# Optimization experiments

Measured on AMD Instinct MI355X. Metric: run time of the kernel, lower is better.

The kernel has to match this reference:

```python
import jax, jax.numpy as jnp
import numpy as np

L = 2        # n_layer
D = 1024     # hidden_size
H = 8        # n_head
DK = D // H  # head_dim = 128
DV = D // H
T = 2048     # max_seq_length
B = 4
INTER = 2816 # fla GatedMLP: int(1024*4*2/3)=2730 rounded up to multiple of 256
EPS = 1e-6


def rmsnorm(x, w):
    return x * jax.lax.rsqrt(jnp.mean(x * x, axis=-1, keepdims=True) + EPS) * w


def l2norm(x):
    return x * jax.lax.rsqrt(jnp.sum(x * x, axis=-1, keepdims=True) + EPS)


def delta_attn(x, Wq, Wk, Wv, Wb, Wo, onorm_w):
    # x: [B, T, D]
    b, t, _ = x.shape
    q = jax.nn.silu((x @ Wq).reshape(b, t, H, DK))
    k = jax.nn.silu((x @ Wk).reshape(b, t, H, DK))
    q = l2norm(q)
    k = l2norm(k)
    v = jax.nn.silu((x @ Wv).reshape(b, t, H, DV))
    beta = jax.nn.sigmoid(x @ Wb) * 2.0  # [B,T,H], allow_neg_eigval=True
    # time-major for scan
    qt = q.transpose(1, 0, 2, 3)  # [T,B,H,DK]
    kt = k.transpose(1, 0, 2, 3)
    vt = v.transpose(1, 0, 2, 3)
    bt = beta.transpose(1, 0, 2)  # [T,B,H]

    def step(S, inps):
        qi, ki, vi, bi = inps
        # delta rule: S_t = S_{t-1} + beta_t * k_t (v_t - S_{t-1}^T k_t)^T
        pred = jnp.einsum('bhkv,bhk->bhv', S, ki)
        S = S + bi[..., None, None] * ki[..., :, None] * (vi - pred)[..., None, :]
        o = jnp.einsum('bhkv,bhk->bhv', S, qi)
        return S, o

    S0 = jnp.zeros((b, H, DK, DV), x.dtype)
    _, o = jax.lax.scan(step, S0, (qt, kt, vt, bt))  # o: [T,B,H,DV]
    o = rmsnorm(o, onorm_w)  # per-head RMSNorm (use_gate=False)
    o = o.transpose(1, 0, 2, 3).reshape(b, t, H * DV)
    return o @ Wo


def setup_inputs() -> dict:
    key = jax.random.key(0)
    ks = jax.random.split(key, 13)
    s = 0.02
    f32 = jnp.float32
    return {
        'input_embeds': jax.random.normal(ks[0], (T, B, D), f32),
        'Wq': jax.random.normal(ks[1], (L, D, D), f32) * s,
        'Wk': jax.random.normal(ks[2], (L, D, D), f32) * s,
        'Wv': jax.random.normal(ks[3], (L, D, D), f32) * s,
        'Wb': jax.random.normal(ks[4], (L, D, H), f32) * s,
        'Wo': jax.random.normal(ks[5], (L, D, D), f32) * s,
        'onorm_w': jnp.ones((L, DV), f32) + jax.random.normal(ks[6], (L, DV), f32) * 0.02,
        'norm1_w': jnp.ones((L, D), f32) + jax.random.normal(ks[7], (L, D), f32) * 0.02,
        'norm2_w': jnp.ones((L, D), f32) + jax.random.normal(ks[8], (L, D), f32) * 0.02,
        'Wg': jax.random.normal(ks[9], (L, D, 2 * INTER), f32) * s,
        'Wd': jax.random.normal(ks[10], (L, INTER, D), f32) * s,
        'final_norm_w': jnp.ones((D,), f32) + jax.random.normal(ks[11], (D,), f32) * 0.02,
    }


def reference(input_embeds, Wq, Wk, Wv, Wb, Wo, onorm_w, norm1_w, norm2_w, Wg, Wd, final_norm_w):
    # wrapper transposes (T,B,D) -> (B,T,D)
    x = input_embeds.transpose(1, 0, 2)
    for l in range(L):
        h = rmsnorm(x, norm1_w[l])
        x = x + delta_attn(h, Wq[l], Wk[l], Wv[l], Wb[l], Wo[l], onorm_w[l])
        h = rmsnorm(x, norm2_w[l])
        gy = h @ Wg[l]
        g, y = jnp.split(gy, 2, axis=-1)
        x = x + (jax.nn.silu(g) * y) @ Wd[l]
    x = rmsnorm(x, final_norm_w)
    return x.transpose(1, 0, 2)  # back to (T,B,D)
```

## Files before the change

kernel.cpp:

```cpp
#include <hip/hip_runtime.h>
#include <hip/hip_bf16.h>
#include <cstdint>


typedef _Float16 f16;
typedef __attribute__((ext_vector_type(8))) _Float16 h8;
typedef __attribute__((ext_vector_type(4))) _Float16 h4;
typedef __attribute__((ext_vector_type(4))) float f4;

#define DEV __device__ __forceinline__

static constexpr int Bb_ = 4;
static constexpr int Hh  = 8;
static constexpr int Dd  = 1024;
static constexpr int Tt  = 2048;
static constexpr int NC  = 32;

DEV float siluf(float x) { return x / (1.f + expf(-x)); }
DEV int swz16(int row, int c) { return (c & 8) | ((c & 7) ^ (row & 7)); }

#define AS1(p) ((const __attribute__((address_space(1))) void*)(uintptr_t)(p))
#define AS3(p) ((__attribute__((address_space(3))) void*)(uint32_t)(uintptr_t)(p))

DEV h8 rd_sw(const f16* T, int row, int chunk) {
  return *(const h8*)(T + (((row << 3) | (chunk ^ (row & 7))) * 8));
}

template<int EPI, int SC>
__global__ __launch_bounds__(512, 2) void gemm2(const f16* __restrict__ A, const f16* __restrict__ Bt,
                                                void* __restrict__ C, const float* __restrict__ rs,
                                                int M, int N, int K, int gx) {
  __shared__ __align__(16) f16 ldsA[2][16384];
  __shared__ __align__(16) f16 ldsB[2][8192];
  const int tid = threadIdx.x, lane = tid & 63, w = tid >> 6;
  const int l15 = lane & 15, l4 = lane >> 4;
  const int wr = w >> 2, wc = w & 3;
  const int nwg = gridDim.x;
  int flat = blockIdx.x;
  if ((nwg & 7) == 0) flat = (flat & 7) * (nwg >> 3) + (flat >> 3);
  const int bx = flat % gx, by = flat / gx;

  const f16* Ab = A + (size_t)by * 256 * K;
  const f16* Bb = Bt + (size_t)bx * 128 * K;
  const int NT = K >> 6;
  f4 acc[8][2] = {};

  const int r0 = tid >> 3;
  const size_t soff0 = (size_t)r0 * K + (size_t)(((tid & 7) ^ (r0 & 7)) * 8);
  const size_t soff1 = soff0 + (size_t)64 * K;
  const int dof = tid * 8;
  auto STG = [&](const f16* base, f16* dst) {
    __builtin_amdgcn_global_load_lds(AS1(base + soff0), AS3(dst + dof), 16, 0, 0);
    __builtin_amdgcn_global_load_lds(AS1(base + soff1), AS3(dst + 4096 + dof), 16, 0, 0);
  };

  STG(Bb, ldsB[0]);
  STG(Ab, ldsA[0]);
  STG(Ab + (size_t)128 * K, ldsA[0] + 8192);
  if (NT > 1) {
    STG(Bb + 64, ldsB[1]);
    asm volatile("s_waitcnt vmcnt(2)");
  } else {
    asm volatile("s_waitcnt vmcnt(0)");
  }
  __builtin_amdgcn_s_barrier();

  for (int t = 0; t < NT; ++t) {
    const int cur = t & 1, nxt = cur ^ 1;
    const f16* cA = ldsA[cur];
    const f16* cB = ldsB[cur];
    h8 b[2][2], aX[2][2], aY[2][2];
#pragma unroll
    for (int cf = 0; cf < 2; ++cf)
#pragma unroll
      for (int ks = 0; ks < 2; ++ks)
        b[cf][ks] = rd_sw(cB, wc * 32 + cf * 16 + l15, ks * 4 + l4);
#pragma unroll
    for (int fr = 0; fr < 2; ++fr)
#pragma unroll
      for (int ks = 0; ks < 2; ++ks)
        aX[fr][ks] = rd_sw(cA, wr * 128 + fr * 16 + l15, ks * 4 + l4);
    if (t + 1 < NT) { STG(Ab + (t + 1) * 64, ldsA[nxt]); STG(Ab + (size_t)128 * K + (t + 1) * 64, ldsA[nxt] + 8192); }
    __builtin_amdgcn_s_setprio(1);
#pragma unroll
    for (int fr = 0; fr < 2; ++fr)
#pragma unroll
      for (int cf = 0; cf < 2; ++cf)
#pragma unroll
        for (int ks = 0; ks < 2; ++ks)
          acc[fr][cf] = __builtin_amdgcn_mfma_f32_16x16x32_f16(aX[fr][ks], b[cf][ks], acc[fr][cf], 0, 0, 0);
#pragma unroll
    for (int fr = 0; fr < 2; ++fr)
#pragma unroll
      for (int ks = 0; ks < 2; ++ks)
        aY[fr][ks] = rd_sw(cA, wr * 128 + 32 + fr * 16 + l15, ks * 4 + l4);
#pragma unroll
    for (int fr = 0; fr < 2; ++fr)
#pragma unroll
      for (int cf = 0; cf < 2; ++cf)
#pragma unroll
        for (int ks = 0; ks < 2; ++ks)
          acc[2 + fr][cf] = __builtin_amdgcn_mfma_f32_16x16x32_f16(aY[fr][ks], b[cf][ks], acc[2 + fr][cf], 0, 0, 0);
    __builtin_amdgcn_s_setprio(0);
    __builtin_amdgcn_s_barrier();
#pragma unroll
    for (int fr = 0; fr < 2; ++fr)
#pragma unroll
      for (int ks = 0; ks < 2; ++ks)
        aX[fr][ks] = rd_sw(cA, wr * 128 + 64 + fr * 16 + l15, ks * 4 + l4);
    if (t + 2 < NT) STG(Bb + (t + 2) * 64, ldsB[cur]);
    __builtin_amdgcn_s_setprio(1);
#pragma unroll
    for (int fr = 0; fr < 2; ++fr)
#pragma unroll
      for (int cf = 0; cf < 2; ++cf)
#pragma unroll
        for (int ks = 0; ks < 2; ++ks)
          acc[4 + fr][cf] = __builtin_amdgcn_mfma_f32_16x16x32_f16(aX[fr][ks], b[cf][ks], acc[4 + fr][cf], 0, 0, 0);
#pragma unroll
    for (int fr = 0; fr < 2; ++fr)
#pragma unroll
      for (int ks = 0; ks < 2; ++ks)
        aY[fr][ks] = rd_sw(cA, wr * 128 + 96 + fr * 16 + l15, ks * 4 + l4);
#pragma unroll
    for (int fr = 0; fr < 2; ++fr)
#pragma unroll
      for (int cf = 0; cf < 2; ++cf)
#pragma unroll
        for (int ks = 0; ks < 2; ++ks)
          acc[6 + fr][cf] = __builtin_amdgcn_mfma_f32_16x16x32_f16(aY[fr][ks], b[cf][ks], acc[6 + fr][cf], 0, 0, 0);
    __builtin_amdgcn_s_setprio(0);
    if (t + 2 < NT)      asm volatile("s_waitcnt vmcnt(2)" ::: "memory");
    else if (t + 1 < NT) asm volatile("s_waitcnt vmcnt(0)" ::: "memory");
    __builtin_amdgcn_s_barrier();
  }

#pragma unroll
  for (int fr = 0; fr < 8; ++fr) {
#pragma unroll
    for (int cf = 0; cf < 2; ++cf) {
      const int row0 = by * 256 + wr * 128 + fr * 16 + l4 * 4;
      const int col = bx * 128 + wc * 32 + cf * 16 + l15;
#pragma unroll
      for (int q = 0; q < 4; ++q) {
        const size_t idx = (size_t)(row0 + q) * N + col;
        float v = acc[fr][cf][q];
        if (SC) v *= rs[row0 + q];
        if (EPI == 1) ((f16*)C)[idx] = (f16)((float)((f16*)C)[idx] + v);
        if (EPI == 2) ((f16*)C)[idx] = (f16)v;
      }
    }
  }
}

__global__ __launch_bounds__(512, 2) void gemmGLU(const f16* __restrict__ A, const f16* __restrict__ WgT,
                                                  const float* __restrict__ rs, f16* __restrict__ my,
                                                  int K, int gx) {
  __shared__ __align__(16) f16 ldsA[2][16384];
  __shared__ __align__(16) f16 ldsG[2][8192];
  __shared__ __align__(16) f16 ldsY[2][8192];
  const int tid = threadIdx.x, lane = tid & 63, w = tid >> 6;
  const int l15 = lane & 15, l4 = lane >> 4;
  const int wr = w >> 2, wc = w & 3;
  const int nwg = gridDim.x;
  int flat = blockIdx.x;
  if ((nwg & 7) == 0) flat = (flat & 7) * (nwg >> 3) + (flat >> 3);
  const int bx = flat % gx, by = flat / gx;

  const f16* Ab = A + (size_t)by * 256 * K;
  const f16* Gb = WgT + (size_t)bx * 128 * K;
  const f16* Yb = WgT + (size_t)(2816 + bx * 128) * K;
  const int NT = K >> 6;
  f4 accG[8][2] = {}, accY[8][2] = {};

  const int r0 = tid >> 3;
  const size_t soff0 = (size_t)r0 * K + (size_t)(((tid & 7) ^ (r0 & 7)) * 8);
  const size_t soff1 = soff0 + (size_t)64 * K;
  const int dof = tid * 8;
  auto STG = [&](const f16* base, f16* dst) {
    __builtin_amdgcn_global_load_lds(AS1(base + soff0), AS3(dst + dof), 16, 0, 0);
    __builtin_amdgcn_global_load_lds(AS1(base + soff1), AS3(dst + 4096 + dof), 16, 0, 0);
  };

  STG(Gb, ldsG[0]);
  STG(Yb, ldsY[0]);
  STG(Ab, ldsA[0]);
  STG(Ab + (size_t)128 * K, ldsA[0] + 8192);
  if (NT > 1) {
    STG(Gb + 64, ldsG[1]);
    STG(Yb + 64, ldsY[1]);
    asm volatile("s_waitcnt vmcnt(4)");
  } else {
    asm volatile("s_waitcnt vmcnt(0)");
  }
  __builtin_amdgcn_s_barrier();

  for (int t = 0; t < NT; ++t) {
    const int cur = t & 1, nxt = cur ^ 1;
    const f16* cA = ldsA[cur];
    h8 bg[2][2], byv[2][2], aX[2][2], aY[2][2];
#pragma unroll
    for (int cf = 0; cf < 2; ++cf)
#pragma unroll
      for (int ks = 0; ks < 2; ++ks) {
        bg[cf][ks] = rd_sw(ldsG[cur], wc * 32 + cf * 16 + l15, ks * 4 + l4);
        byv[cf][ks] = rd_sw(ldsY[cur], wc * 32 + cf * 16 + l15, ks * 4 + l4);
      }
#pragma unroll
    for (int fr = 0; fr < 2; ++fr)
#pragma unroll
      for (int ks = 0; ks < 2; ++ks)
        aX[fr][ks] = rd_sw(cA, wr * 128 + fr * 16 + l15, ks * 4 + l4);
    if (t + 1 < NT) { STG(Ab + (t + 1) * 64, ldsA[nxt]); STG(Ab + (size_t)128 * K + (t + 1) * 64, ldsA[nxt] + 8192); }
    __builtin_amdgcn_s_setprio(1);
#pragma unroll
    for (int fr = 0; fr < 2; ++fr)
#pragma unroll
      for (int cf = 0; cf < 2; ++cf)
#pragma unroll
        for (int ks = 0; ks < 2; ++ks) {
          accG[fr][cf] = __builtin_amdgcn_mfma_f32_16x16x32_f16(aX[fr][ks], bg[cf][ks], accG[fr][cf], 0, 0, 0);
          accY[fr][cf] = __builtin_amdgcn_mfma_f32_16x16x32_f16(aX[fr][ks], byv[cf][ks], accY[fr][cf], 0, 0, 0);
        }
#pragma unroll
    for (int fr = 0; fr < 2; ++fr)
#pragma unroll
      for (int ks = 0; ks < 2; ++ks)
        aY[fr][ks] = rd_sw(cA, wr * 128 + 32 + fr * 16 + l15, ks * 4 + l4);
#pragma unroll
    for (int fr = 0; fr < 2; ++fr)
#pragma unroll
      for (int cf = 0; cf < 2; ++cf)
#pragma unroll
        for (int ks = 0; ks < 2; ++ks) {
          accG[2 + fr][cf] = __builtin_amdgcn_mfma_f32_16x16x32_f16(aY[fr][ks], bg[cf][ks], accG[2 + fr][cf], 0, 0, 0);
          accY[2 + fr][cf] = __builtin_amdgcn_mfma_f32_16x16x32_f16(aY[fr][ks], byv[cf][ks], accY[2 + fr][cf], 0, 0, 0);
        }
    __builtin_amdgcn_s_setprio(0);
    __builtin_amdgcn_s_barrier();
#pragma unroll
    for (int fr = 0; fr < 2; ++fr)
#pragma unroll
      for (int ks = 0; ks < 2; ++ks)
        aX[fr][ks] = rd_sw(cA, wr * 128 + 64 + fr * 16 + l15, ks * 4 + l4);
    if (t + 2 < NT) { STG(Gb + (t + 2) * 64, ldsG[cur]); STG(Yb + (t + 2) * 64, ldsY[cur]); }
    __builtin_amdgcn_s_setprio(1);
#pragma unroll
    for (int fr = 0; fr < 2; ++fr)
#pragma unroll
      for (int cf = 0; cf < 2; ++cf)
#pragma unroll
        for (int ks = 0; ks < 2; ++ks) {
          accG[4 + fr][cf] = __builtin_amdgcn_mfma_f32_16x16x32_f16(aX[fr][ks], bg[cf][ks], accG[4 + fr][cf], 0, 0, 0);
          accY[4 + fr][cf] = __builtin_amdgcn_mfma_f32_16x16x32_f16(aX[fr][ks], byv[cf][ks], accY[4 + fr][cf], 0, 0, 0);
        }
#pragma unroll
    for (int fr = 0; fr < 2; ++fr)
#pragma unroll
      for (int ks = 0; ks < 2; ++ks)
        aY[fr][ks] = rd_sw(cA, wr * 128 + 96 + fr * 16 + l15, ks * 4 + l4);
#pragma unroll
    for (int fr = 0; fr < 2; ++fr)
#pragma unroll
      for (int cf = 0; cf < 2; ++cf)
#pragma unroll
        for (int ks = 0; ks < 2; ++ks) {
          accG[6 + fr][cf] = __builtin_amdgcn_mfma_f32_16x16x32_f16(aY[fr][ks], bg[cf][ks], accG[6 + fr][cf], 0, 0, 0);
          accY[6 + fr][cf] = __builtin_amdgcn_mfma_f32_16x16x32_f16(aY[fr][ks], byv[cf][ks], accY[6 + fr][cf], 0, 0, 0);
        }
    __builtin_amdgcn_s_setprio(0);
    if (t + 2 < NT)      asm volatile("s_waitcnt vmcnt(4)" ::: "memory");
    else if (t + 1 < NT) asm volatile("s_waitcnt vmcnt(0)" ::: "memory");
    __builtin_amdgcn_s_barrier();
  }

#pragma unroll
  for (int fr = 0; fr < 8; ++fr) {
#pragma unroll
    for (int cf = 0; cf < 2; ++cf) {
      const int row0 = by * 256 + wr * 128 + fr * 16 + l4 * 4;
      const int col = bx * 128 + wc * 32 + cf * 16 + l15;
#pragma unroll
      for (int q = 0; q < 4; ++q) {
        const float s = rs[row0 + q];
        my[(size_t)(row0 + q) * 2816 + col] = (f16)(siluf(s * accG[fr][cf][q]) * (s * accY[fr][cf][q]));
      }
    }
  }
}

__global__ __launch_bounds__(256) void cvt_k(const float* __restrict__ in, f16* __restrict__ out) {
  const size_t i = ((size_t)blockIdx.x * 256 + threadIdx.x) * 8;
  const float4 a = *(const float4*)(in + i);
  const float4 b = *(const float4*)(in + i + 4);
  h8 o = {(f16)a.x, (f16)a.y, (f16)a.z, (f16)a.w, (f16)b.x, (f16)b.y, (f16)b.z, (f16)b.w};
  *(h8*)(out + i) = o;
}

__global__ __launch_bounds__(256) void rowscale_k(const f16* __restrict__ x, float* __restrict__ rs) {
  const int tid = threadIdx.x, lane = tid & 63, wv = tid >> 6;
  const int r = blockIdx.x * 4 + wv;
  const f16* row = x + (size_t)r * 1024 + lane * 16;
  const h8 v0 = *(const h8*)(row);
  const h8 v1 = *(const h8*)(row + 8);
  float ss = 0.f;
#pragma unroll
  for (int e = 0; e < 8; ++e) {
    const float a = (float)v0[e], b = (float)v1[e];
    ss += a * a + b * b;
  }
#pragma unroll
  for (int m = 1; m < 64; m <<= 1) ss += __shfl_xor(ss, m);
  if (lane == 0) rs[r] = rsqrtf(ss * (1.f / 1024.f) + 1e-6f);
}

__global__ __launch_bounds__(256) void rmsnorm_f(const f16* __restrict__ x, const float* __restrict__ w,
                                                 float* __restrict__ out) {
  const int r = blockIdx.x, tid = threadIdx.x;
  const h4 xv = *(const h4*)(x + (size_t)r * 1024 + tid * 4);
  const float v0 = (float)xv[0], v1 = (float)xv[1], v2 = (float)xv[2], v3 = (float)xv[3];
  float ss = v0 * v0 + v1 * v1 + v2 * v2 + v3 * v3;
#pragma unroll
  for (int m = 1; m < 64; m <<= 1) ss += __shfl_xor(ss, m);
  __shared__ float red[4];
  if ((tid & 63) == 0) red[tid >> 6] = ss;
  __syncthreads();
  const float scale = rsqrtf((red[0] + red[1] + red[2] + red[3]) * (1.f / 1024.f) + 1e-6f);
  const float4 w4 = *(const float4*)(w + tid * 4);
  *(float4*)(out + (size_t)r * 1024 + tid * 4) =
      make_float4(v0 * scale * w4.x, v1 * scale * w4.y, v2 * scale * w4.z, v3 * scale * w4.w);
}

__global__ __launch_bounds__(256) void qkv_epi(const f16* __restrict__ qkv, f16* __restrict__ qb,
                                               f16* __restrict__ kb, f16* __restrict__ vb) {
  const int r = blockIdx.x, tid = threadIdx.x;
  const int head = tid >> 5, l32 = tid & 31;
  const int i = (r >> 2) & 63;
  const size_t src = (size_t)r * 3072 + head * 128 + l32 * 4;
  {
    const h4 v = *(const h4*)(qkv + src);
    float s0 = siluf((float)v[0]), s1 = siluf((float)v[1]), s2 = siluf((float)v[2]), s3 = siluf((float)v[3]);
    float ss = s0 * s0 + s1 * s1 + s2 * s2 + s3 * s3;
#pragma unroll
    for (int m = 1; m <= 16; m <<= 1) ss += __shfl_xor(ss, m);
    const float sc = rsqrtf(ss + 1e-6f);
    h4 o = {(f16)(s0 * sc), (f16)(s1 * sc), (f16)(s2 * sc), (f16)(s3 * sc)};
    const int c = l32 >> 1, off = (l32 & 1) * 4;
    *(h4*)(qb + (size_t)r * 1024 + head * 128 + swz16(i, c) * 8 + off) = o;
  }
  {
    const h4 v = *(const h4*)(qkv + src + 1024);
    float s0 = siluf((float)v[0]), s1 = siluf((float)v[1]), s2 = siluf((float)v[2]), s3 = siluf((float)v[3]);
    float ss = s0 * s0 + s1 * s1 + s2 * s2 + s3 * s3;
#pragma unroll
    for (int m = 1; m <= 16; m <<= 1) ss += __shfl_xor(ss, m);
    const float sc = rsqrtf(ss + 1e-6f);
    h4 o = {(f16)(s0 * sc), (f16)(s1 * sc), (f16)(s2 * sc), (f16)(s3 * sc)};
    const int c = l32 >> 1, off = (l32 & 1) * 4;
    *(h4*)(kb + (size_t)r * 1024 + head * 128 + swz16(i, c) * 8 + off) = o;
  }
  {
    const h4 v = *(const h4*)(qkv + (size_t)r * 3072 + 2048 + tid * 4);
    h4 o = {(f16)siluf((float)v[0]), (f16)siluf((float)v[1]), (f16)siluf((float)v[2]), (f16)siluf((float)v[3])};
    const int hd = tid >> 5, dh = (tid & 31) * 4;
    const int c = dh >> 3, off = dh & 7;
    *(h4*)(vb + (size_t)r * 1024 + hd * 128 + swz16(i, c) * 8 + off) = o;
  }
}

__global__ __launch_bounds__(256) void onorm_k(const f16* __restrict__ o, const float* __restrict__ w,
                                               f16* __restrict__ ob) {
  const int r = blockIdx.x, tid = threadIdx.x;
  const int head = tid >> 5, l32 = tid & 31;
  const size_t base = (size_t)r * 1024 + head * 128 + l32 * 4;
  const h4 xv = *(const h4*)(o + base);
  const float v0 = (float)xv[0], v1 = (float)xv[1], v2 = (float)xv[2], v3 = (float)xv[3];
  float ss = v0 * v0 + v1 * v1 + v2 * v2 + v3 * v3;
#pragma unroll
  for (int m = 1; m <= 16; m <<= 1) ss += __shfl_xor(ss, m);
  const float sc = rsqrtf(ss * (1.f / 128.f) + 1e-6f);
  const float4 w4 = *(const float4*)(w + l32 * 4);
  h4 out = {(f16)(v0 * sc * w4.x), (f16)(v1 * sc * w4.y), (f16)(v2 * sc * w4.z), (f16)(v3 * sc * w4.w)};
  *(h4*)(ob + base) = out;
}

__global__ __launch_bounds__(256) void beta_k(const f16* __restrict__ x, const float* __restrict__ Wb2,
                                              const float* __restrict__ rs, float* __restrict__ beta) {
  const int tid = threadIdx.x, lane = tid & 63, wv = tid >> 6;
  const int r = blockIdx.x * 4 + wv;
  const f16* row = x + (size_t)r * 1024 + lane * 16;
  const h8 v0 = *(const h8*)(row);
  const h8 v1 = *(const h8*)(row + 8);
  const float* wb = Wb2 + (size_t)(lane * 16) * 8;
  float acc[8] = {};
#pragma unroll
  for (int e = 0; e < 8; ++e) {
    const float x0 = (float)v0[e], x1 = (float)v1[e];
    const float4 w0a = *(const float4*)(wb + e * 8);
    const float4 w0b = *(const float4*)(wb + e * 8 + 4);
    const float4 w1a = *(const float4*)(wb + (e + 8) * 8);
    const float4 w1b = *(const float4*)(wb + (e + 8) * 8 + 4);
    acc[0] += x0 * w0a.x + x1 * w1a.x;  acc[1] += x0 * w0a.y + x1 * w1a.y;
    acc[2] += x0 * w0a.z + x1 * w1a.z;  acc[3] += x0 * w0a.w + x1 * w1a.w;
    acc[4] += x0 * w0b.x + x1 * w1b.x;  acc[5] += x0 * w0b.y + x1 * w1b.y;
    acc[6] += x0 * w0b.z + x1 * w1b.z;  acc[7] += x0 * w0b.w + x1 * w1b.w;
  }
#pragma unroll
  for (int j = 0; j < 8; ++j)
#pragma unroll
    for (int m = 1; m < 64; m <<= 1) acc[j] += __shfl_xor(acc[j], m);
  if (lane == 0) {
    const float s = rs[r];
#pragma unroll
    for (int j = 0; j < 8; ++j) beta[(size_t)r * 8 + j] = 2.f / (1.f + expf(-acc[j] * s));
  }
}

template<int FOLD>
__global__ __launch_bounds__(256) void transpose_k(const float* __restrict__ W, const float* __restrict__ rw,
                                                   f16* __restrict__ Wt, int K, int N) {
  __shared__ float tile[32][33];
  const int n0 = blockIdx.x * 32, k0 = blockIdx.y * 32;
  const int tx = threadIdx.x & 31, ty = threadIdx.x >> 5;
#pragma unroll
  for (int i = 0; i < 32; i += 8) {
    float v = W[(size_t)(k0 + ty + i) * N + n0 + tx];
    if (FOLD) v *= rw[k0 + ty + i];
    tile[ty + i][tx] = v;
  }
  __syncthreads();
#pragma unroll
  for (int i = 0; i < 32; i += 8) Wt[(size_t)(n0 + ty + i) * K + k0 + tx] = (f16)tile[tx][ty + i];
}

__global__ __launch_bounds__(256) void bweight_k(const float* __restrict__ Wb, const float* __restrict__ n1w,
                                                 float* __restrict__ Wb2) {
  const int idx = blockIdx.x * 256 + threadIdx.x;
  Wb2[idx] = Wb[idx] * n1w[idx >> 3];
}

__global__ void fill_k(float* p, int n, float v) {
  const int i = blockIdx.x * 256 + threadIdx.x;
  if (i < n) p[i] = v;
}

DEV f4 mm16(const f16* A, int as, const f16* B, f4 c, int l15, int l4) {
  h4 a = *(const h4*)(A + l15 * as + l4 * 4);
  h4 b = *(const h4*)(B + l15 * 20 + l4 * 4);
  return __builtin_amdgcn_mfma_f32_16x16x16f16(a, b, c, 0, 0, 0);
}
DEV void wr_T(f16* slot, f4 acc, int l15, int l4, float sgn) {
  h4 v = {(f16)(sgn * acc[0]), (f16)(sgn * acc[1]), (f16)(sgn * acc[2]), (f16)(sgn * acc[3])};
  *(h4*)(slot + l15 * 20 + l4 * 4) = v;
}
DEV void wr_Tb(f16* Tb, int bi, int bj, f4 acc, const float* betas, int l15, int l4, float sgn) {
  const float bc = betas[bj * 16 + l15];
#pragma unroll
  for (int q = 0; q < 4; ++q)
    Tb[(bi * 16 + l4 * 4 + q) * 72 + bj * 16 + l15] = (f16)(sgn * acc[q] * bc);
}

__global__ __launch_bounds__(256) void phaseA(const f16* __restrict__ kb, const f16* __restrict__ qb,
                                              const f16* __restrict__ vb, const float* __restrict__ beta,
                                              f16* __restrict__ wbuf, f16* __restrict__ utbuf,
                                              f16* __restrict__ pbuf, f16* __restrict__ ktbuf) {
  const int blk = blockIdx.x;
  const int c = blk >> 5, bh = blk & 31;
  const int b = bh >> 3, h = bh & 7;
  const int tid = threadIdx.x, lane = tid & 63, wv = tid >> 6;
  const int l15 = lane & 15, l4 = lane >> 4;

  __shared__ __align__(16) f16 Ks[64 * 128];
  __shared__ __align__(16) f16 QVs[64 * 128];
  __shared__ __align__(16) f16 Abuf[64 * 68];
  __shared__ __align__(16) f16 Dr[4][16 * 20];
  __shared__ __align__(16) f16 Dt[4][16 * 20];
  __shared__ __align__(16) f16 Tp[3][16 * 20];
  __shared__ __align__(16) f16 Xp[3][16 * 20];
  __shared__ __align__(16) f16 Tb[64 * 72];
  __shared__ float betas[64];

  const size_t rowstr = (size_t)Bb_ * Dd;
  const size_t gbase = ((size_t)(c * 64) * Bb_ + b) * Dd + h * 128;

#pragma unroll
  for (int i = 0; i < 4; ++i) {
    const int ch = tid + i * 256;
    const int rr = ch >> 4, kc = ch & 15;
    *(h8*)(Ks + ch * 8) = *(const h8*)(kb + gbase + (size_t)rr * rowstr + kc * 8);
    *(h8*)(QVs + ch * 8) = *(const h8*)(qb + gbase + (size_t)rr * rowstr + kc * 8);
  }
  for (int i = tid; i < 64 * 72; i += 256) Tb[i] = (f16)0.f;
  if (tid < 64) betas[tid] = beta[((size_t)(c * 64 + tid) * Bb_ + b) * Hh + h];
  __syncthreads();

  f4 accS[4] = {}, accP[4] = {};
  const int arow = wv * 16 + l15;
#pragma unroll
  for (int kc = 0; kc < 4; ++kc) {
    const int c4 = kc * 4 + l4;
    const h8 aK = *(const h8*)(Ks + arow * 128 + swz16(arow, c4) * 8);
    const h8 aQ = *(const h8*)(QVs + arow * 128 + swz16(arow, c4) * 8);
#pragma unroll
    for (int f = 0; f < 4; ++f) {
      const int brow = f * 16 + l15;
      const h8 bK = *(const h8*)(Ks + brow * 128 + swz16(brow, c4) * 8);
      accS[f] = __builtin_amdgcn_mfma_f32_16x16x32_f16(aK, bK, accS[f], 0, 0, 0);
      accP[f] = __builtin_amdgcn_mfma_f32_16x16x32_f16(aQ, bK, accP[f], 0, 0, 0);
    }
  }
  const size_t pbase = (((size_t)bh * NC + c) * 64) * 64;
#pragma unroll
  for (int f = 0; f < 4; ++f) {
#pragma unroll
    for (int q = 0; q < 4; ++q) {
      const int i = wv * 16 + l4 * 4 + q;
      const int j = f * 16 + l15;
      Abuf[i * 68 + j] = (f16)((j < i) ? betas[i] * accS[f][q] : 0.f);
      pbuf[pbase + (size_t)i * 64 + j] = (f16)((j <= i) ? accP[f][q] : 0.f);
    }
  }
  __syncthreads();

#pragma unroll
  for (int i = 0; i < 4; ++i) {
    const int ch = tid + i * 256;
    const int rr = ch >> 4, kc = ch & 15;
    *(h8*)(QVs + ch * 8) = *(const h8*)(vb + gbase + (size_t)rr * rowstr + kc * 8);
  }

  {
    const int bi = wv;
    const int cc = l15;
    const f16* Ad = Abuf + (bi * 16) * 68 + bi * 16;
    float t[16];
    t[0] = (cc == 0) ? 1.f : 0.f;
#pragma unroll
    for (int i = 1; i < 16; ++i) {
      float s = (cc == i) ? 1.f : 0.f;
#pragma unroll
      for (int j = 0; j < i; ++j) s -= (float)Ad[i * 68 + j] * t[j];
      t[i] = s;
    }
    if (lane < 16) {
#pragma unroll
      for (int j4 = 0; j4 < 4; ++j4) {
        h4 v = {(f16)t[j4 * 4], (f16)t[j4 * 4 + 1], (f16)t[j4 * 4 + 2], (f16)t[j4 * 4 + 3]};
        *(h4*)(&Dt[bi][cc * 20 + j4 * 4]) = v;
      }
      const float bc = betas[bi * 16 + cc];
#pragma unroll
      for (int j = 0; j < 16; ++j) {
        Dr[bi][j * 20 + cc] = (f16)t[j];
        Tb[(bi * 16 + j) * 72 + bi * 16 + cc] = (f16)(t[j] * bc);
      }
    }
  }
  __syncthreads();

  const f16* AB10 = Abuf + 16 * 68 + 0;
  const f16* AB20 = Abuf + 32 * 68 + 0;
  const f16* AB21 = Abuf + 32 * 68 + 16;
  const f16* AB30 = Abuf + 48 * 68 + 0;
  const f16* AB31 = Abuf + 48 * 68 + 16;
  const f16* AB32 = Abuf + 48 * 68 + 32;
  f4 z = {};
  f4 x20, x30;

  if (wv == 0) wr_T(Xp[0], mm16(AB10, 68, Dt[0], z, l15, l4), l15, l4, 1.f);
  if (wv == 1) wr_T(Xp[1], mm16(AB21, 68, Dt[1], z, l15, l4), l15, l4, 1.f);
  if (wv == 2) wr_T(Xp[2], mm16(AB32, 68, Dt[2], z, l15, l4), l15, l4, 1.f);
  if (wv == 3) x20 = mm16(AB20, 68, Dt[0], z, l15, l4);
  __syncthreads();
  if (wv == 0) { f4 r = mm16(Dr[1], 20, Xp[0], z, l15, l4); wr_T(Tp[0], r, l15, l4, -1.f); wr_Tb(Tb, 1, 0, r, betas, l15, l4, -1.f); }
  if (wv == 1) { f4 r = mm16(Dr[2], 20, Xp[1], z, l15, l4); wr_T(Tp[1], r, l15, l4, -1.f); wr_Tb(Tb, 2, 1, r, betas, l15, l4, -1.f); }
  if (wv == 2) { f4 r = mm16(Dr[3], 20, Xp[2], z, l15, l4); wr_Tb(Tb, 3, 2, r, betas, l15, l4, -1.f); }
  if (wv == 3) x30 = mm16(AB30, 68, Dt[0], z, l15, l4);
  __syncthreads();
  if (wv == 3) wr_T(Xp[0], mm16(AB21, 68, Tp[0], x20, l15, l4), l15, l4, 1.f);
  if (wv == 1) { f4 r = mm16(AB31, 68, Dt[1], z, l15, l4); r = mm16(AB32, 68, Tp[1], r, l15, l4); wr_T(Xp[1], r, l15, l4, 1.f); }
  __syncthreads();
  if (wv == 3) { f4 r = mm16(Dr[2], 20, Xp[0], z, l15, l4); wr_T(Tp[2], r, l15, l4, -1.f); wr_Tb(Tb, 2, 0, r, betas, l15, l4, -1.f); }
  if (wv == 1) { f4 r = mm16(Dr[3], 20, Xp[1], z, l15, l4); wr_Tb(Tb, 3, 1, r, betas, l15, l4, -1.f); }
  __syncthreads();
  if (wv == 3) { f4 r = mm16(AB31, 68, Tp[0], x30, l15, l4); r = mm16(AB32, 68, Tp[2], r, l15, l4); wr_T(Xp[2], r, l15, l4, 1.f); }
  __syncthreads();
  if (wv == 3) { f4 r = mm16(Dr[3], 20, Xp[2], z, l15, l4); wr_Tb(Tb, 3, 0, r, betas, l15, l4, -1.f); }
  __syncthreads();

  const size_t wub = ((size_t)bh * NC + c) * 8192;
  const int koff = l4 * 8;
  f4 wacc[8] = {}, uacc[8] = {};
#pragma unroll
  for (int kc = 0; kc < 2; ++kc) {
    const h8 aT = *(const h8*)(Tb + (wv * 16 + l15) * 72 + kc * 32 + koff);
#pragma unroll
    for (int f = 0; f < 8; ++f) {
      const int d = f * 16 + l15, cD = d >> 3, d7 = d & 7;
      h8 bK, bV;
#pragma unroll
      for (int j = 0; j < 8; ++j) {
        const int t2 = kc * 32 + koff + j;
        const int pos = t2 * 128 + swz16(t2, cD) * 8 + d7;
        bK[j] = Ks[pos];
        bV[j] = QVs[pos];
      }
      wacc[f] = __builtin_amdgcn_mfma_f32_16x16x32_f16(aT, bK, wacc[f], 0, 0, 0);
      uacc[f] = __builtin_amdgcn_mfma_f32_16x16x32_f16(aT, bV, uacc[f], 0, 0, 0);
    }
  }
#pragma unroll
  for (int f = 0; f < 8; ++f) {
    const int d = f * 16 + l15, cD = d >> 3, d7 = d & 7;
#pragma unroll
    for (int q = 0; q < 4; ++q) {
      const int i = wv * 16 + l4 * 4 + q;
      wbuf[wub + (size_t)i * 128 + swz16(i, cD) * 8 + d7] = (f16)wacc[f][q];
    }
    h4 uv = {(f16)uacc[f][0], (f16)uacc[f][1], (f16)uacc[f][2], (f16)uacc[f][3]};
    *(h4*)(utbuf + wub + (size_t)d * 64 + wv * 16 + l4 * 4) = uv;
  }

#pragma unroll
  for (int i2 = 0; i2 < 4; ++i2) {
    const int ch = tid + i2 * 256;
    const int dp = ch & 127, c2 = ch >> 7;
    h8 v;
#pragma unroll
    for (int j = 0; j < 8; ++j) {
      const int i = c2 * 8 + j;
      v[j] = Ks[i * 128 + swz16(i, dp >> 3) * 8 + (dp & 7)];
    }
    *(h8*)(ktbuf + wub + (size_t)dp * 64 + (c2 ^ (dp & 7)) * 8) = v;
  }
}

__global__ __launch_bounds__(256) void phaseB(const f16* __restrict__ qb, const f16* __restrict__ ktbuf,
                                              const f16* __restrict__ wbuf, const f16* __restrict__ utbuf,
                                              const f16* __restrict__ pbuf, f16* __restrict__ obuf) {
  const int blk = blockIdx.x;
  const int bh = blk >> 2, g = blk & 3;
  const int b = bh >> 3, h = bh & 7;
  const int tid = threadIdx.x, lane = tid & 63, wv = tid >> 6;
  const int l15 = lane & 15, l4 = lane >> 4;

  __shared__ __align__(16) f16 Ws[2][8192];
  __shared__ __align__(16) f16 Qs[2][8192];
  __shared__ __align__(16) f16 Kts[2][8192];
  __shared__ __align__(16) f16 Rt[32 * 72];
  __shared__ __align__(16) f16 Ms[32 * 136];

  for (int i = tid; i < 32 * 136; i += 256) Ms[i] = (f16)0.f;
  f4 macc[2][2] = {};

  const int arow = wv * 16 + l15;
  const int koff = l4 * 8;

  auto STAGE = [&](int c2, int buf) {
#pragma unroll
    for (int i = 0; i < 4; ++i) {
      const int ch = tid + i * 256;
      const size_t tb = ((size_t)bh * NC + c2) * 8192;
      __builtin_amdgcn_global_load_lds(AS1(wbuf + tb + ch * 8), AS3(Ws[buf] + ch * 8), 16, 0, 0);
      __builtin_amdgcn_global_load_lds(AS1(ktbuf + tb + ch * 8), AS3(Kts[buf] + ch * 8), 16, 0, 0);
      const int rr = ch >> 4, kc2 = ch & 15;
      __builtin_amdgcn_global_load_lds(AS1(qb + ((size_t)((c2 * 64 + rr) * 4 + b)) * 1024 + h * 128 + kc2 * 8),
                                       AS3(Qs[buf] + ch * 8), 16, 0, 0);
    }
  };

  STAGE(0, 0);
  asm volatile("s_waitcnt vmcnt(0)" ::: "memory");
  __builtin_amdgcn_s_barrier();

  for (int c = 0; c < NC; ++c) {
    const int cur = c & 1, nxt = cur ^ 1;
    const size_t pcb = ((size_t)bh * NC + c) * 4096;
    const h8 aP0 = *(const h8*)(pbuf + pcb + arow * 64 + koff);
    const h8 aP1 = *(const h8*)(pbuf + pcb + arow * 64 + 32 + koff);
    const size_t ucb = ((size_t)bh * NC + c) * 8192;
    const h4 u0 = *(const h4*)(utbuf + ucb + (size_t)(g * 32 + l15) * 64 + wv * 16 + l4 * 4);
    const h4 u1 = *(const h4*)(utbuf + ucb + (size_t)(g * 32 + 16 + l15) * 64 + wv * 16 + l4 * 4);
    asm volatile("s_waitcnt vmcnt(4)" ::: "memory");
    asm volatile("s_waitcnt lgkmcnt(0)" ::: "memory");
    __builtin_amdgcn_s_barrier();
    if (c + 1 < NC) STAGE(c + 1, nxt);

    f4 accR[2] = {}, accO[2] = {};
    __builtin_amdgcn_s_setprio(1);
#pragma unroll
    for (int kc = 0; kc < 4; ++kc) {
      const int c4 = kc * 4 + l4;
      const h8 aW = *(const h8*)(Ws[cur] + arow * 128 + swz16(arow, c4) * 8);
      const h8 aQ = *(const h8*)(Qs[cur] + arow * 128 + swz16(arow, c4) * 8);
#pragma unroll
      for (int f = 0; f < 2; ++f) {
        const h8 bM = *(const h8*)(Ms + (f * 16 + l15) * 136 + kc * 32 + koff);
        accR[f] = __builtin_amdgcn_mfma_f32_16x16x32_f16(aW, bM, accR[f], 0, 0, 0);
        accO[f] = __builtin_amdgcn_mfma_f32_16x16x32_f16(aQ, bM, accO[f], 0, 0, 0);
      }
    }
    __builtin_amdgcn_s_setprio(0);
    if (c + 1 < NC) asm volatile("s_waitcnt vmcnt(12)" ::: "memory");
    else            asm volatile("s_waitcnt vmcnt(0)" ::: "memory");
#pragma unroll
    for (int f = 0; f < 2; ++f) {
      const h4 uu = f ? u1 : u0;
      h4 rw;
#pragma unroll
      for (int q = 0; q < 4; ++q) {
        const float rv = (float)uu[q] - accR[f][q];
        accR[f][q] = rv;
        rw[q] = (f16)rv;
      }
      *(h4*)(Rt + (f * 16 + l15) * 72 + wv * 16 + l4 * 4) = rw;
    }
    asm volatile("s_waitcnt lgkmcnt(0)" ::: "memory");
    __builtin_amdgcn_s_barrier();

#pragma unroll
    for (int kc = 0; kc < 2; ++kc) {
      const h8 aP = kc ? aP1 : aP0;
#pragma unroll
      for (int f = 0; f < 2; ++f) {
        const h8 bR = *(const h8*)(Rt + (f * 16 + l15) * 72 + kc * 32 + koff);
        accO[f] = __builtin_amdgcn_mfma_f32_16x16x32_f16(aP, bR, accO[f], 0, 0, 0);
      }
    }
#pragma unroll
    for (int f = 0; f < 2; ++f)
#pragma unroll
      for (int q = 0; q < 4; ++q) {
        const int i = wv * 16 + l4 * 4 + q;
        const int cc = f * 16 + l15;
        obuf[((size_t)(c * 64 + i) * Bb_ + b) * Dd + h * 128 + g * 32 + cc] = (f16)accO[f][q];
      }

#pragma unroll
    for (int kc = 0; kc < 2; ++kc) {
      const h8 aR0 = *(const h8*)(Rt + l15 * 72 + kc * 32 + koff);
      const h8 aR1 = *(const h8*)(Rt + (16 + l15) * 72 + kc * 32 + koff);
#pragma unroll
      for (int cf = 0; cf < 2; ++cf) {
        const int kcol = wv * 32 + cf * 16 + l15;
        const int c2 = kc * 4 + l4;
        const h8 bKv = *(const h8*)(Kts[cur] + kcol * 64 + (c2 ^ (kcol & 7)) * 8);
        macc[0][cf] = __builtin_amdgcn_mfma_f32_16x16x32_f16(aR0, bKv, macc[0][cf], 0, 0, 0);
        macc[1][cf] = __builtin_amdgcn_mfma_f32_16x16x32_f16(aR1, bKv, macc[1][cf], 0, 0, 0);
      }
    }
#pragma unroll
    for (int rf = 0; rf < 2; ++rf)
#pragma unroll
      for (int cf = 0; cf < 2; ++cf)
#pragma unroll
        for (int q = 0; q < 4; ++q) {
          const int cr = rf * 16 + l4 * 4 + q;
          const int kcol = wv * 32 + cf * 16 + l15;
          Ms[cr * 136 + kcol] = (f16)macc[rf][cf][q];
        }
  }
}

extern "C" void kernel_launch(void* const* d_in, const int* in_sizes, int n_in,
                              void* d_out, int out_size, void* d_ws, size_t ws_size,
                              hipStream_t stream) {
  (void)in_sizes; (void)n_in;
  const float* input = (const float*)d_in[0];
  const float* Wq = (const float*)d_in[1];
  const float* Wk = (const float*)d_in[2];
  const float* Wv = (const float*)d_in[3];
  const float* Wb = (const float*)d_in[4];
  const float* Wo = (const float*)d_in[5];
  const float* onw = (const float*)d_in[6];
  const float* n1w = (const float*)d_in[7];
  const float* n2w = (const float*)d_in[8];
  const float* Wg = (const float*)d_in[9];
  const float* Wd = (const float*)d_in[10];
  const float* fnw = (const float*)d_in[11];

  char* ws = (char*)d_ws;
  size_t off = 0;
  auto alloc = [&](size_t bytes) { void* p = ws + off; off += (bytes + 255) & ~(size_t)255; return p; };
  const size_t RD = 8192ull * 1024ull;
  f16*  x     = (f16*)alloc(RD * 2);
  f16*  qb    = (f16*)alloc(RD * 2);
  f16*  kbuf  = (f16*)alloc(RD * 2);
  f16*  vbuf  = (f16*)alloc(RD * 2);
  float* beta = (float*)alloc(8192ull * 8 * 4);
  float* rs   = (float*)alloc(8192ull * 4);
  float* Wb2  = (float*)alloc(1024ull * 8 * 4);
  f16*  wbuf  = (f16*)alloc(RD * 2);
  f16*  utbuf = (f16*)alloc(RD * 2);
  f16*  ktbuf = (f16*)alloc(RD * 2);
  f16*  pbuf  = (f16*)alloc(32ull * 32 * 64 * 64 * 2);
  char* arena = (char*)alloc(3 * RD * 2);
  f16*  WqkvT = (f16*)alloc(3072ull * 1024 * 2);
  f16*  WoT   = (f16*)alloc(1024ull * 1024 * 2);
  f16*  WgT   = (f16*)alloc(5632ull * 1024 * 2);
  f16*  WdT   = (f16*)alloc(1024ull * 2816 * 2);
  if (off > ws_size) {
    fill_k<<<(out_size + 255) / 256, 256, 0, stream>>>((float*)d_out, out_size, 1.0e6f);
    return;
  }
  f16* qkvraw = (f16*)arena;
  f16* obuf = (f16*)arena;
  f16* my = qb;
  f16* ob = wbuf;

  cvt_k<<<4096, 256, 0, stream>>>(input, x);

  for (int l = 0; l < 2; ++l) {
    const size_t o2 = (size_t)l * 1024 * 1024;
    transpose_k<1><<<dim3(32, 32), 256, 0, stream>>>(Wq + o2, n1w + l * 1024, WqkvT, 1024, 1024);
    transpose_k<1><<<dim3(32, 32), 256, 0, stream>>>(Wk + o2, n1w + l * 1024, WqkvT + 1024ull * 1024, 1024, 1024);
    transpose_k<1><<<dim3(32, 32), 256, 0, stream>>>(Wv + o2, n1w + l * 1024, WqkvT + 2048ull * 1024, 1024, 1024);
    transpose_k<0><<<dim3(32, 32), 256, 0, stream>>>(Wo + o2, nullptr, WoT, 1024, 1024);
    transpose_k<1><<<dim3(176, 32), 256, 0, stream>>>(Wg + (size_t)l * 1024 * 5632, n2w + l * 1024, WgT, 1024, 5632);
    transpose_k<0><<<dim3(32, 88), 256, 0, stream>>>(Wd + (size_t)l * 2816 * 1024, nullptr, WdT, 2816, 1024);
    bweight_k<<<32, 256, 0, stream>>>(Wb + (size_t)l * 1024 * 8, n1w + l * 1024, Wb2);

    rowscale_k<<<2048, 256, 0, stream>>>(x, rs);
    gemm2<2, 1><<<32 * 24, 512, 0, stream>>>(x, WqkvT, qkvraw, rs, 8192, 3072, 1024, 24);
    beta_k<<<2048, 256, 0, stream>>>(x, Wb2, rs, beta);
    qkv_epi<<<8192, 256, 0, stream>>>(qkvraw, qb, kbuf, vbuf);
    phaseA<<<1024, 256, 0, stream>>>(kbuf, qb, vbuf, beta, wbuf, utbuf, pbuf, ktbuf);
    phaseB<<<128, 256, 0, stream>>>(qb, ktbuf, wbuf, utbuf, pbuf, obuf);
    onorm_k<<<8192, 256, 0, stream>>>(obuf, onw + l * 128, ob);
    gemm2<1, 0><<<32 * 8, 512, 0, stream>>>(ob, WoT, x, nullptr, 8192, 1024, 1024, 8);

    rowscale_k<<<2048, 256, 0, stream>>>(x, rs);
    gemmGLU<<<32 * 22, 512, 0, stream>>>(x, WgT, rs, my, 1024, 22);
    gemm2<1, 0><<<32 * 8, 512, 0, stream>>>(my, WdT, x, nullptr, 8192, 1024, 2816, 8);
  }
  rmsnorm_f<<<8192, 256, 0, stream>>>(x, fnw, (float*)d_out);
}
```

Baseline: 989.2 us.

## Fuse QKV epilogue into GEMM and split phaseB across more blocks

Adds a gemmQKV kernel that applies row scaling, SiLU, per-head L2 normalization and the swizzled scatter to q/k/v directly in the GEMM epilogue. This removes the separate qkv_epi pass and the raw QKV intermediate round trip through memory. PhaseB now splits each (batch, head) state into 8 column groups of 16 instead of 4 groups of 32, launching 256 blocks instead of 128, with a reordered block index. That raises parallelism in the scan at the cost of recomputing the shared W/Q/P loads per group and doing thinner MFMA work per block.

```diff
diff --git a/kernel.cpp b/kernel.cpp
--- a/kernel.cpp
+++ b/kernel.cpp
@@ -153,6 +153,170 @@
   }
 }
 
+__global__ __launch_bounds__(512, 2) void gemmQKV(const f16* __restrict__ A, const f16* __restrict__ Bt,
+                                                  const float* __restrict__ rs, f16* __restrict__ qb,
+                                                  f16* __restrict__ kb, f16* __restrict__ vb,
+                                                  int K, int gx) {
+  __shared__ __align__(16) f16 ldsA[2][16384];
+  __shared__ __align__(16) f16 ldsB[2][8192];
+  __shared__ float ps[4][256];
+  const int tid = threadIdx.x, lane = tid & 63, w = tid >> 6;
+  const int l15 = lane & 15, l4 = lane >> 4;
+  const int wr = w >> 2, wc = w & 3;
+  const int nwg = gridDim.x;
+  int flat = blockIdx.x;
+  if ((nwg & 7) == 0) flat = (flat & 7) * (nwg >> 3) + (flat >> 3);
+  const int bx = flat % gx, by = flat / gx;
+
+  const f16* Ab = A + (size_t)by * 256 * K;
+  const f16* Bb = Bt + (size_t)bx * 128 * K;
+  const int NT = K >> 6;
+  f4 acc[8][2] = {};
+
+  const int r0 = tid >> 3;
+  const size_t soff0 = (size_t)r0 * K + (size_t)(((tid & 7) ^ (r0 & 7)) * 8);
+  const size_t soff1 = soff0 + (size_t)64 * K;
+  const int dof = tid * 8;
+  auto STG = [&](const f16* base, f16* dst) {
+    __builtin_amdgcn_global_load_lds(AS1(base + soff0), AS3(dst + dof), 16, 0, 0);
+    __builtin_amdgcn_global_load_lds(AS1(base + soff1), AS3(dst + 4096 + dof), 16, 0, 0);
+  };
+
+  STG(Bb, ldsB[0]);
+  STG(Ab, ldsA[0]);
+  STG(Ab + (size_t)128 * K, ldsA[0] + 8192);
+  if (NT > 1) {
+    STG(Bb + 64, ldsB[1]);
+    asm volatile("s_waitcnt vmcnt(2)");
+  } else {
+    asm volatile("s_waitcnt vmcnt(0)");
+  }
+  __builtin_amdgcn_s_barrier();
+
+  for (int t = 0; t < NT; ++t) {
+    const int cur = t & 1, nxt = cur ^ 1;
+    const f16* cA = ldsA[cur];
+    const f16* cB = ldsB[cur];
+    h8 b[2][2], aX[2][2], aY[2][2];
+#pragma unroll
+    for (int cf = 0; cf < 2; ++cf)
+#pragma unroll
+      for (int ks = 0; ks < 2; ++ks)
+        b[cf][ks] = rd_sw(cB, wc * 32 + cf * 16 + l15, ks * 4 + l4);
+#pragma unroll
+    for (int fr = 0; fr < 2; ++fr)
+#pragma unroll
+      for (int ks = 0; ks < 2; ++ks)
+        aX[fr][ks] = rd_sw(cA, wr * 128 + fr * 16 + l15, ks * 4 + l4);
+    if (t + 1 < NT) { STG(Ab + (t + 1) * 64, ldsA[nxt]); STG(Ab + (size_t)128 * K + (t + 1) * 64, ldsA[nxt] + 8192); }
+    __builtin_amdgcn_s_setprio(1);
+#pragma unroll
+    for (int fr = 0; fr < 2; ++fr)
+#pragma unroll
+      for (int cf = 0; cf < 2; ++cf)
+#pragma unroll
+        for (int ks = 0; ks < 2; ++ks)
+          acc[fr][cf] = __builtin_amdgcn_mfma_f32_16x16x32_f16(aX[fr][ks], b[cf][ks], acc[fr][cf], 0, 0, 0);
+#pragma unroll
+    for (int fr = 0; fr < 2; ++fr)
+#pragma unroll
+      for (int ks = 0; ks < 2; ++ks)
+        aY[fr][ks] = rd_sw(cA, wr * 128 + 32 + fr * 16 + l15, ks * 4 + l4);
+#pragma unroll
+    for (int fr = 0; fr < 2; ++fr)
+#pragma unroll
+      for (int cf = 0; cf < 2; ++cf)
+#pragma unroll
+        for (int ks = 0; ks < 2; ++ks)
+          acc[2 + fr][cf] = __builtin_amdgcn_mfma_f32_16x16x32_f16(aY[fr][ks], b[cf][ks], acc[2 + fr][cf], 0, 0, 0);
+    __builtin_amdgcn_s_setprio(0);
+    __builtin_amdgcn_s_barrier();
+#pragma unroll
+    for (int fr = 0; fr < 2; ++fr)
+#pragma unroll
+      for (int ks = 0; ks < 2; ++ks)
+        aX[fr][ks] = rd_sw(cA, wr * 128 + 64 + fr * 16 + l15, ks * 4 + l4);
+    if (t + 2 < NT) STG(Bb + (t + 2) * 64, ldsB[cur]);
+    __builtin_amdgcn_s_setprio(1);
+#pragma unroll
+    for (int fr = 0; fr < 2; ++fr)
+#pragma unroll
+      for (int cf = 0; cf < 2; ++cf)
+#pragma unroll
+        for (int ks = 0; ks < 2; ++ks)
+          acc[4 + fr][cf] = __builtin_amdgcn_mfma_f32_16x16x32_f16(aX[fr][ks], b[cf][ks], acc[4 + fr][cf], 0, 0, 0);
+#pragma unroll
+    for (int fr = 0; fr < 2; ++fr)
+#pragma unroll
+      for (int ks = 0; ks < 2; ++ks)
+        aY[fr][ks] = rd_sw(cA, wr * 128 + 96 + fr * 16 + l15, ks * 4 + l4);
+#pragma unroll
+    for (int fr = 0; fr < 2; ++fr)
+#pragma unroll
+      for (int cf = 0; cf < 2; ++cf)
+#pragma unroll
+        for (int ks = 0; ks < 2; ++ks)
+          acc[6 + fr][cf] = __builtin_amdgcn_mfma_f32_16x16x32_f16(aY[fr][ks], b[cf][ks], acc[6 + fr][cf], 0, 0, 0);
+    __builtin_amdgcn_s_setprio(0);
+    if (t + 2 < NT)      asm volatile("s_waitcnt vmcnt(2)" ::: "memory");
+    else if (t + 1 < NT) asm volatile("s_waitcnt vmcnt(0)" ::: "memory");
+    __builtin_amdgcn_s_barrier();
+  }
+
+#pragma unroll
+  for (int fr = 0; fr < 8; ++fr)
+#pragma unroll
+    for (int q = 0; q < 4; ++q) {
+      const int grow = by * 256 + wr * 128 + fr * 16 + l4 * 4 + q;
+      const float s = rs[grow];
+#pragma unroll
+      for (int cf = 0; cf < 2; ++cf)
+        acc[fr][cf][q] = siluf(s * acc[fr][cf][q]);
+    }
+  if (bx < 16) {
+    float sq[8][4];
+#pragma unroll
+    for (int fr = 0; fr < 8; ++fr)
+#pragma unroll
+      for (int q = 0; q < 4; ++q) {
+        float v = acc[fr][0][q] * acc[fr][0][q] + acc[fr][1][q] * acc[fr][1][q];
+#pragma unroll
+        for (int m = 1; m < 16; m <<= 1) v += __shfl_xor(v, m);
+        sq[fr][q] = v;
+      }
+    if (l15 == 0) {
+#pragma unroll
+      for (int fr = 0; fr < 8; ++fr)
+#pragma unroll
+        for (int q = 0; q < 4; ++q)
+          ps[wc][wr * 128 + fr * 16 + l4 * 4 + q] = sq[fr][q];
+    }
+    __syncthreads();
+#pragma unroll
+    for (int fr = 0; fr < 8; ++fr)
+#pragma unroll
+      for (int q = 0; q < 4; ++q) {
+        const int rl = wr * 128 + fr * 16 + l4 * 4 + q;
+        const float sc = rsqrtf(ps[0][rl] + ps[1][rl] + ps[2][rl] + ps[3][rl] + 1e-6f);
+#pragma unroll
+        for (int cf = 0; cf < 2; ++cf) acc[fr][cf][q] *= sc;
+      }
+  }
+  f16* dst = (bx < 8) ? qb : ((bx < 16) ? kb : vb);
+  const int head = bx & 7;
+#pragma unroll
+  for (int fr = 0; fr < 8; ++fr)
+#pragma unroll
+    for (int cf = 0; cf < 2; ++cf)
+#pragma unroll
+      for (int q = 0; q < 4; ++q) {
+        const int grow = by * 256 + wr * 128 + fr * 16 + l4 * 4 + q;
+        const int i = (grow >> 2) & 63;
+        const int dh = wc * 32 + cf * 16 + l15;
+        dst[(size_t)grow * 1024 + head * 128 + swz16(i, dh >> 3) * 8 + (dh & 7)] = (f16)acc[fr][cf][q];
+      }
+}
+
 __global__ __launch_bounds__(512, 2) void gemmGLU(const f16* __restrict__ A, const f16* __restrict__ WgT,
                                                   const float* __restrict__ rs, f16* __restrict__ my,
                                                   int K, int gx) {
@@ -331,43 +495,6 @@
       make_float4(v0 * scale * w4.x, v1 * scale * w4.y, v2 * scale * w4.z, v3 * scale * w4.w);
 }
 
-__global__ __launch_bounds__(256) void qkv_epi(const f16* __restrict__ qkv, f16* __restrict__ qb,
-                                               f16* __restrict__ kb, f16* __restrict__ vb) {
-  const int r = blockIdx.x, tid = threadIdx.x;
-  const int head = tid >> 5, l32 = tid & 31;
-  const int i = (r >> 2) & 63;
-  const size_t src = (size_t)r * 3072 + head * 128 + l32 * 4;
-  {
-    const h4 v = *(const h4*)(qkv + src);
-    float s0 = siluf((float)v[0]), s1 = siluf((float)v[1]), s2 = siluf((float)v[2]), s3 = siluf((float)v[3]);
-    float ss = s0 * s0 + s1 * s1 + s2 * s2 + s3 * s3;
-#pragma unroll
-    for (int m = 1; m <= 16; m <<= 1) ss += __shfl_xor(ss, m);
-    const float sc = rsqrtf(ss + 1e-6f);
-    h4 o = {(f16)(s0 * sc), (f16)(s1 * sc), (f16)(s2 * sc), (f16)(s3 * sc)};
-    const int c = l32 >> 1, off = (l32 & 1) * 4;
-    *(h4*)(qb + (size_t)r * 1024 + head * 128 + swz16(i, c) * 8 + off) = o;
-  }
-  {
-    const h4 v = *(const h4*)(qkv + src + 1024);
-    float s0 = siluf((float)v[0]), s1 = siluf((float)v[1]), s2 = siluf((float)v[2]), s3 = siluf((float)v[3]);
-    float ss = s0 * s0 + s1 * s1 + s2 * s2 + s3 * s3;
-#pragma unroll
-    for (int m = 1; m <= 16; m <<= 1) ss += __shfl_xor(ss, m);
-    const float sc = rsqrtf(ss + 1e-6f);
-    h4 o = {(f16)(s0 * sc), (f16)(s1 * sc), (f16)(s2 * sc), (f16)(s3 * sc)};
-    const int c = l32 >> 1, off = (l32 & 1) * 4;
-    *(h4*)(kb + (size_t)r * 1024 + head * 128 + swz16(i, c) * 8 + off) = o;
-  }
-  {
-    const h4 v = *(const h4*)(qkv + (size_t)r * 3072 + 2048 + tid * 4);
-    h4 o = {(f16)siluf((float)v[0]), (f16)siluf((float)v[1]), (f16)siluf((float)v[2]), (f16)siluf((float)v[3])};
-    const int hd = tid >> 5, dh = (tid & 31) * 4;
-    const int c = dh >> 3, off = dh & 7;
-    *(h4*)(vb + (size_t)r * 1024 + hd * 128 + swz16(i, c) * 8 + off) = o;
-  }
-}
-
 __global__ __launch_bounds__(256) void onorm_k(const f16* __restrict__ o, const float* __restrict__ w,
                                                f16* __restrict__ ob) {
   const int r = blockIdx.x, tid = threadIdx.x;
@@ -639,7 +766,7 @@
                                               const f16* __restrict__ wbuf, const f16* __restrict__ utbuf,
                                               const f16* __restrict__ pbuf, f16* __restrict__ obuf) {
   const int blk = blockIdx.x;
-  const int bh = blk >> 2, g = blk & 3;
+  const int bh = blk & 31, g = blk >> 5;
   const int b = bh >> 3, h = bh & 7;
   const int tid = threadIdx.x, lane = tid & 63, wv = tid >> 6;
   const int l15 = lane & 15, l4 = lane >> 4;
@@ -647,11 +774,11 @@
   __shared__ __align__(16) f16 Ws[2][8192];
   __shared__ __align__(16) f16 Qs[2][8192];
   __shared__ __align__(16) f16 Kts[2][8192];
-  __shared__ __align__(16) f16 Rt[32 * 72];
-  __shared__ __align__(16) f16 Ms[32 * 136];
-
-  for (int i = tid; i < 32 * 136; i += 256) Ms[i] = (f16)0.f;
-  f4 macc[2][2] = {};
+  __shared__ __align__(16) f16 Rt[16 * 72];
+  __shared__ __align__(16) f16 Ms[16 * 136];
+
+  for (int i = tid; i < 16 * 136; i += 256) Ms[i] = (f16)0.f;
+  f4 macc2[2] = {};
 
   const int arow = wv * 16 + l15;
   const int koff = l4 * 8;
@@ -679,41 +806,34 @@
     const h8 aP0 = *(const h8*)(pbuf + pcb + arow * 64 + koff);
     const h8 aP1 = *(const h8*)(pbuf + pcb + arow * 64 + 32 + koff);
     const size_t ucb = ((size_t)bh * NC + c) * 8192;
-    const h4 u0 = *(const h4*)(utbuf + ucb + (size_t)(g * 32 + l15) * 64 + wv * 16 + l4 * 4);
-    const h4 u1 = *(const h4*)(utbuf + ucb + (size_t)(g * 32 + 16 + l15) * 64 + wv * 16 + l4 * 4);
-    asm volatile("s_waitcnt vmcnt(4)" ::: "memory");
+    const h4 u0 = *(const h4*)(utbuf + ucb + (size_t)(g * 16 + l15) * 64 + wv * 16 + l4 * 4);
+    asm volatile("s_waitcnt vmcnt(3)" ::: "memory");
     asm volatile("s_waitcnt lgkmcnt(0)" ::: "memory");
     __builtin_amdgcn_s_barrier();
     if (c + 1 < NC) STAGE(c + 1, nxt);
 
-    f4 accR[2] = {}, accO[2] = {};
+    f4 accR = {}, accO = {};
     __builtin_amdgcn_s_setprio(1);
 #pragma unroll
     for (int kc = 0; kc < 4; ++kc) {
       const int c4 = kc * 4 + l4;
       const h8 aW = *(const h8*)(Ws[cur] + arow * 128 + swz16(arow, c4) * 8);
       const h8 aQ = *(const h8*)(Qs[cur] + arow * 128 + swz16(arow, c4) * 8);
-#pragma unroll
-      for (int f = 0; f < 2; ++f) {
-        const h8 bM = *(const h8*)(Ms + (f * 16 + l15) * 136 + kc * 32 + koff);
-        accR[f] = __builtin_amdgcn_mfma_f32_16x16x32_f16(aW, bM, accR[f], 0, 0, 0);
-        accO[f] = __builtin_amdgcn_mfma_f32_16x16x32_f16(aQ, bM, accO[f], 0, 0, 0);
-      }
+      const h8 bM = *(const h8*)(Ms + l15 * 136 + kc * 32 + koff);
+      accR = __builtin_amdgcn_mfma_f32_16x16x32_f16(aW, bM, accR, 0, 0, 0);
+      accO = __builtin_amdgcn_mfma_f32_16x16x32_f16(aQ, bM, accO, 0, 0, 0);
     }
     __builtin_amdgcn_s_setprio(0);
     if (c + 1 < NC) asm volatile("s_waitcnt vmcnt(12)" ::: "memory");
     else            asm volatile("s_waitcnt vmcnt(0)" ::: "memory");
-#pragma unroll
-    for (int f = 0; f < 2; ++f) {
-      const h4 uu = f ? u1 : u0;
+    {
       h4 rw;
 #pragma unroll
       for (int q = 0; q < 4; ++q) {
-        const float rv = (float)uu[q] - accR[f][q];
-        accR[f][q] = rv;
+        const float rv = (float)u0[q] - accR[q];
         rw[q] = (f16)rv;
       }
-      *(h4*)(Rt + (f * 16 + l15) * 72 + wv * 16 + l4 * 4) = rw;
+      *(h4*)(Rt + l15 * 72 + wv * 16 + l4 * 4) = rw;
     }
     asm volatile("s_waitcnt lgkmcnt(0)" ::: "memory");
     __builtin_amdgcn_s_barrier();
@@ -721,44 +841,34 @@
 #pragma unroll
     for (int kc = 0; kc < 2; ++kc) {
       const h8 aP = kc ? aP1 : aP0;
-#pragma unroll
-      for (int f = 0; f < 2; ++f) {
-        const h8 bR = *(const h8*)(Rt + (f * 16 + l15) * 72 + kc * 32 + koff);
-        accO[f] = __builtin_amdgcn_mfma_f32_16x16x32_f16(aP, bR, accO[f], 0, 0, 0);
-      }
-    }
-#pragma unroll
-    for (int f = 0; f < 2; ++f)
-#pragma unroll
-      for (int q = 0; q < 4; ++q) {
-        const int i = wv * 16 + l4 * 4 + q;
-        const int cc = f * 16 + l15;
-        obuf[((size_t)(c * 64 + i) * Bb_ + b) * Dd + h * 128 + g * 32 + cc] = (f16)accO[f][q];
-      }
+      const h8 bR = *(const h8*)(Rt + l15 * 72 + kc * 32 + koff);
+      accO = __builtin_amdgcn_mfma_f32_16x16x32_f16(aP, bR, accO, 0, 0, 0);
+    }
+#pragma unroll
+    for (int q = 0; q < 4; ++q) {
+      const int i = wv * 16 + l4 * 4 + q;
+      obuf[((size_t)(c * 64 + i) * Bb_ + b) * Dd + h * 128 + g * 16 + l15] = (f16)accO[q];
+    }
 
 #pragma unroll
     for (int kc = 0; kc < 2; ++kc) {
       const h8 aR0 = *(const h8*)(Rt + l15 * 72 + kc * 32 + koff);
-      const h8 aR1 = *(const h8*)(Rt + (16 + l15) * 72 + kc * 32 + koff);
 #pragma unroll
       for (int cf = 0; cf < 2; ++cf) {
         const int kcol = wv * 32 + cf * 16 + l15;
         const int c2 = kc * 4 + l4;
         const h8 bKv = *(const h8*)(Kts[cur] + kcol * 64 + (c2 ^ (kcol & 7)) * 8);
-        macc[0][cf] = __builtin_amdgcn_mfma_f32_16x16x32_f16(aR0, bKv, macc[0][cf], 0, 0, 0);
-        macc[1][cf] = __builtin_amdgcn_mfma_f32_16x16x32_f16(aR1, bKv, macc[1][cf], 0, 0, 0);
-      }
-    }
-#pragma unroll
-    for (int rf = 0; rf < 2; ++rf)
-#pragma unroll
-      for (int cf = 0; cf < 2; ++cf)
-#pragma unroll
-        for (int q = 0; q < 4; ++q) {
-          const int cr = rf * 16 + l4 * 4 + q;
-          const int kcol = wv * 32 + cf * 16 + l15;
-          Ms[cr * 136 + kcol] = (f16)macc[rf][cf][q];
-        }
+        macc2[cf] = __builtin_amdgcn_mfma_f32_16x16x32_f16(aR0, bKv, macc2[cf], 0, 0, 0);
+      }
+    }
+#pragma unroll
+    for (int cf = 0; cf < 2; ++cf)
+#pragma unroll
+      for (int q = 0; q < 4; ++q) {
+        const int cr = l4 * 4 + q;
+        const int kcol = wv * 32 + cf * 16 + l15;
+        Ms[cr * 136 + kcol] = (f16)macc2[cf][q];
+      }
   }
 }
 
@@ -803,7 +913,6 @@
     fill_k<<<(out_size + 255) / 256, 256, 0, stream>>>((float*)d_out, out_size, 1.0e6f);
     return;
   }
-  f16* qkvraw = (f16*)arena;
   f16* obuf = (f16*)arena;
   f16* my = qb;
   f16* ob = wbuf;
@@ -821,11 +930,10 @@
     bweight_k<<<32, 256, 0, stream>>>(Wb + (size_t)l * 1024 * 8, n1w + l * 1024, Wb2);
 
     rowscale_k<<<2048, 256, 0, stream>>>(x, rs);
-    gemm2<2, 1><<<32 * 24, 512, 0, stream>>>(x, WqkvT, qkvraw, rs, 8192, 3072, 1024, 24);
+    gemmQKV<<<32 * 24, 512, 0, stream>>>(x, WqkvT, rs, qb, kbuf, vbuf, 1024, 24);
     beta_k<<<2048, 256, 0, stream>>>(x, Wb2, rs, beta);
-    qkv_epi<<<8192, 256, 0, stream>>>(qkvraw, qb, kbuf, vbuf);
     phaseA<<<1024, 256, 0, stream>>>(kbuf, qb, vbuf, beta, wbuf, utbuf, pbuf, ktbuf);
-    phaseB<<<128, 256, 0, stream>>>(qb, ktbuf, wbuf, utbuf, pbuf, obuf);
+    phaseB<<<256, 256, 0, stream>>>(qb, ktbuf, wbuf, utbuf, pbuf, obuf);
     onorm_k<<<8192, 256, 0, stream>>>(obuf, onw + l * 128, ob);
     gemm2<1, 0><<<32 * 8, 512, 0, stream>>>(ob, WoT, x, nullptr, 8192, 1024, 1024, 8);
 
```

After: 943.6 us. -4.6%, faster.
